# Performance work log

Measured on AMD Instinct MI355X. Metric: run time of the kernel, lower is better.

Reference implementation:

```python
import jax, jax.numpy as jnp
import numpy as np

NEG_BIG = -9e15

def setup_inputs() -> dict:
    key = jax.random.key(0)
    k1, k2, k3, k4 = jax.random.split(key, 4)
    B, N, C, D = 8, 2048, 128, 128
    x = jax.random.normal(k1, (B, N, C), dtype=jnp.float32)
    adj = jax.random.randint(k2, (N, N), 0, 2, dtype=jnp.int32)
    W = jax.random.normal(k3, (D, C), dtype=jnp.float32) * (1.0 / np.sqrt(C))
    a = jax.random.normal(k4, (1, 2 * D), dtype=jnp.float32) * (1.0 / np.sqrt(2 * D))
    return {"x": x, "adj": adj, "W": W, "a": a}

def reference(x, adj, W, a):
    # Wh: [B,N,D]
    Wh = jnp.einsum('bnc,dc->bnd', x, W)
    D = Wh.shape[-1]
    a1, a2 = a[0, :D], a[0, D:]
    # e[b,i,j] = leakyrelu(a1.Wh_i + a2.Wh_j)  (algebraic split of cat([Wh_i,Wh_j]) @ a)
    f1 = Wh @ a1  # [B,N]
    f2 = Wh @ a2  # [B,N]
    e = jax.nn.leaky_relu(f1[:, :, None] + f2[:, None, :], negative_slope=0.2)  # [B,N,N]
    e = jnp.where(adj[None] > 0, e, NEG_BIG)
    attention = jax.nn.softmax(e, axis=-1)
    h_prime = jnp.einsum('bij,bjd->bid', attention, Wh)
    return jax.nn.elu(h_prime)
```

## Files before the change

### kernel.cpp

```cpp
#include <hip/hip_runtime.h>
#include <hip/hip_bf16.h>
#include <math.h>

#define BB 8
#define NN 2048
#define CC 128
#define DD 128

typedef __attribute__((ext_vector_type(8))) short short8;
typedef __attribute__((ext_vector_type(4))) float f32x4;

static __device__ __forceinline__ unsigned short f2bf(float f) {
    __hip_bfloat16 h = __float2bfloat16(f);
    return *reinterpret_cast<unsigned short*>(&h);
}
static __device__ __forceinline__ float bf2f(unsigned short u) {
    __hip_bfloat16 h = *reinterpret_cast<__hip_bfloat16*>(&u);
    return __bfloat162float(h);
}

#define PACKB 256
__global__ __launch_bounds__(256) void prep_wh_kernel(
    const int* __restrict__ adj, unsigned int* __restrict__ padj,
    const float* __restrict__ x, const float* __restrict__ W,
    const float* __restrict__ a,
    unsigned short* __restrict__ WhbT,
    float* __restrict__ f1, unsigned int* __restrict__ EGp)
{
    __shared__ unsigned short Whs[128 * 136];
    __shared__ unsigned short Wls[128 * 136];
    const int bx  = blockIdx.x;
    const int tid = threadIdx.x;

    if (bx < PACKB) {
        const int wid = bx * 256 + tid;
        #pragma unroll
        for (int rep = 0; rep < 2; ++rep) {
            const int word = wid + rep * 65536;
            const int4* src = (const int4*)adj + (size_t)word * 8;
            unsigned int m = 0;
            #pragma unroll
            for (int k = 0; k < 8; ++k) {
                int4 v = src[k];
                m |= (v.x > 0 ? 1u : 0u) << (k * 4);
                m |= (v.y > 0 ? 1u : 0u) << (k * 4 + 1);
                m |= (v.z > 0 ? 1u : 0u) << (k * 4 + 2);
                m |= (v.w > 0 ? 1u : 0u) << (k * 4 + 3);
            }
            padj[word] = m;
        }
        return;
    }

    const int g  = bx - PACKB;
    const int b  = g & 7;
    const int n0 = (g >> 3) * 64;

    #pragma unroll
    for (int k = 0; k < 16; ++k) {
        const int e   = tid + 256 * k;
        float4 wv = *(const float4*)&W[e * 4];
        const int row = e >> 5;
        const int col = (e & 31) * 4;
        ushort4 hv, lv;
        hv.x = f2bf(wv.x); lv.x = f2bf(wv.x - bf2f(hv.x));
        hv.y = f2bf(wv.y); lv.y = f2bf(wv.y - bf2f(hv.y));
        hv.z = f2bf(wv.z); lv.z = f2bf(wv.z - bf2f(hv.z));
        hv.w = f2bf(wv.w); lv.w = f2bf(wv.w - bf2f(hv.w));
        *(ushort4*)&Whs[row * 136 + col] = hv;
        *(ushort4*)&Wls[row * 136 + col] = lv;
    }
    __syncthreads();

    const int w    = tid >> 6;
    const int lane = tid & 63;
    const int fr   = lane & 15, fk = lane >> 4;
    const int n    = n0 + w * 16 + fr;

    short8 bh[4], bl[4];
    const float* xrow = &x[((size_t)(b * NN) + n) * CC];
    #pragma unroll
    for (int ks = 0; ks < 4; ++ks) {
        float xv[8];
        *(float4*)&xv[0] = *(const float4*)&xrow[(ks * 4 + fk) * 8];
        *(float4*)&xv[4] = *(const float4*)&xrow[(ks * 4 + fk) * 8 + 4];
        #pragma unroll
        for (int e = 0; e < 8; ++e) {
            unsigned short h = f2bf(xv[e]);
            bh[ks][e] = (short)h;
            bl[ks][e] = (short)f2bf(xv[e] - bf2f(h));
        }
    }

    f32x4 acc[8];
    #pragma unroll
    for (int dt = 0; dt < 8; ++dt) acc[dt] = (f32x4){0.f, 0.f, 0.f, 0.f};

    #pragma unroll
    for (int dt = 0; dt < 8; ++dt) {
        #pragma unroll
        for (int ks = 0; ks < 4; ++ks) {
            const int off = (dt * 16 + fr) * 136 + (ks * 4 + fk) * 8;
            short8 aH = *(const short8*)&Whs[off];
            short8 aL = *(const short8*)&Wls[off];
            acc[dt] = __builtin_amdgcn_mfma_f32_16x16x32_bf16(aH, bh[ks], acc[dt], 0, 0, 0);
            acc[dt] = __builtin_amdgcn_mfma_f32_16x16x32_bf16(aH, bl[ks], acc[dt], 0, 0, 0);
            acc[dt] = __builtin_amdgcn_mfma_f32_16x16x32_bf16(aL, bh[ks], acc[dt], 0, 0, 0);
        }
    }

    float p1 = 0.f, p2 = 0.f;
    #pragma unroll
    for (int dt = 0; dt < 8; ++dt) {
        #pragma unroll
        for (int r = 0; r < 4; ++r) {
            const int d = dt * 16 + fk * 4 + r;
            p1 += acc[dt][r] * a[d];
            p2 += acc[dt][r] * a[DD + d];
        }
    }
    p1 += __shfl_xor(p1, 16); p1 += __shfl_xor(p1, 32);
    p2 += __shfl_xor(p2, 16); p2 += __shfl_xor(p2, 32);
    if (fk == 0) {
        f1[b * NN + n] = p1;
        unsigned short e2 = f2bf(__expf(p2));
        unsigned short g2 = f2bf(__expf(0.2f * p2));
        EGp[b * NN + n] = (unsigned int)e2 | ((unsigned int)g2 << 16);
    }

    #pragma unroll
    for (int dt = 0; dt < 8; ++dt) {
        #pragma unroll
        for (int r = 0; r < 4; ++r) {
            const int d = dt * 16 + fk * 4 + r;
            WhbT[((size_t)(b * 128 + d)) * NN + n] = f2bf(acc[dt][r]);
        }
    }
}

__global__ __launch_bounds__(256) void gat_kernel(
    const unsigned short* __restrict__ WhbT,
    const unsigned int* __restrict__ padj,
    const float* __restrict__ f1,
    const unsigned int* __restrict__ EGp,
    float* __restrict__ out)
{
    constexpr int NC = NN / 64;
    __shared__ __align__(16) unsigned char smem[41216];
    unsigned short* Bs0 = (unsigned short*)smem;
    unsigned short* Bs1 = (unsigned short*)(smem + 16384);
    unsigned short* Ps0 = (unsigned short*)(smem + 32768);
    unsigned short* Ps1 = (unsigned short*)(smem + 36864);
    float* Srow = (float*)(smem + 40960);
    float* Sred = (float*)(smem + 41088);
    float* T    = (float*)smem;

    const int tid  = threadIdx.x;
    const int gblk = blockIdx.x;
    const int b    = gblk & 7;
    const int i0   = (gblk >> 3) * 32;

    const int prow = tid >> 3;
    const int pjb  = tid & 7;
    const float f1r = f1[b * NN + i0 + prow];
    const float E1r = __expf(f1r);
    const float G1r = __expf(0.2f * f1r);
    const int psw = ((pjb ^ (prow & 7)) << 3);
    const unsigned int* padjRow = padj + (size_t)(i0 + prow) * 64;
    const unsigned int* egRow   = EGp + (size_t)b * NN + pjb * 8;

    const int w    = tid >> 6;
    const int lane = tid & 63;
    const int fr   = lane & 15;
    const int fk   = lane >> 4;
    f32x4 acc00 = {0.f,0.f,0.f,0.f}, acc01 = {0.f,0.f,0.f,0.f};
    f32x4 acc10 = {0.f,0.f,0.f,0.f}, acc11 = {0.f,0.f,0.f,0.f};
    float s_part = 0.f;

    const size_t wbase = (size_t)b * 128 * NN;
    const int g0 = tid,       gd0 = g0 >> 3, gj0 = (g0 & 7) * 8;
    const int g1 = tid + 256, gd1 = g1 >> 3, gj1 = (g1 & 7) * 8;
    const int g2 = tid + 512, gd2 = g2 >> 3, gj2 = (g2 & 7) * 8;
    const int g3 = tid + 768, gd3 = g3 >> 3, gj3 = (g3 & 7) * 8;
    const int sw0 = gd0 * 64 + ((((g0) & 7) ^ (gd0 & 7)) << 3);
    const int sw1 = gd1 * 64 + ((((g1) & 7) ^ (gd1 & 7)) << 3);
    const int sw2 = gd2 * 64 + ((((g2) & 7) ^ (gd2 & 7)) << 3);
    const int sw3 = gd3 * 64 + ((((g3) & 7) ^ (gd3 & 7)) << 3);

    uint4 brA0, brA1, brA2, brA3, brB0, brB1, brB2, brB3;
    uint4 egA0, egA1, egB0, egB1;
    unsigned int pwA, pwB;

#define LOADSET(s, c) do {                                                   \
        br##s##0 = *(const uint4*)&WhbT[wbase + (size_t)gd0 * NN + (c) * 64 + gj0]; \
        br##s##1 = *(const uint4*)&WhbT[wbase + (size_t)gd1 * NN + (c) * 64 + gj1]; \
        br##s##2 = *(const uint4*)&WhbT[wbase + (size_t)gd2 * NN + (c) * 64 + gj2]; \
        br##s##3 = *(const uint4*)&WhbT[wbase + (size_t)gd3 * NN + (c) * 64 + gj3]; \
        pw##s    = padjRow[(c) * 2 + (pjb >> 2)];                            \
        eg##s##0 = *(const uint4*)(egRow + (c) * 64);                        \
        eg##s##1 = *(const uint4*)(egRow + (c) * 64 + 4);                    \
    } while (0)

#define PSTAGE(Bsb, Psb, s) do {                                             \
        unsigned int egw[8];                                                 \
        *(uint4*)&egw[0] = eg##s##0; *(uint4*)&egw[4] = eg##s##1;            \
        unsigned int pbits = (pw##s >> ((pjb & 3) << 3)) & 0xffu;            \
        unsigned short pks[8];                                               \
        float ssum = 0.f;                                                    \
        _Pragma("unroll")                                                    \
        for (int e = 0; e < 8; ++e) {                                        \
            float e2 = bf2f((unsigned short)(egw[e] & 0xffffu));             \
            float g2 = bf2f((unsigned short)(egw[e] >> 16));                 \
            float mv = E1r * e2;                                             \
            float gg = G1r * g2;                                             \
            float wv = fmaxf(mv, gg);                                        \
            wv = ((pbits >> e) & 1u) ? wv : 0.f;                             \
            unsigned short bw = f2bf(wv);                                    \
            pks[e] = bw;                                                     \
            ssum += bf2f(bw);                                                \
        }                                                                    \
        s_part += ssum;                                                      \
        *(uint4*)&Bsb[sw0] = br##s##0;                                       \
        *(uint4*)&Bsb[sw1] = br##s##1;                                       \
        *(uint4*)&Bsb[sw2] = br##s##2;                                       \
        *(uint4*)&Bsb[sw3] = br##s##3;                                       \
        uint4 pv;                                                            \
        pv.x = (unsigned int)pks[0] | ((unsigned int)pks[1] << 16);          \
        pv.y = (unsigned int)pks[2] | ((unsigned int)pks[3] << 16);          \
        pv.z = (unsigned int)pks[4] | ((unsigned int)pks[5] << 16);          \
        pv.w = (unsigned int)pks[6] | ((unsigned int)pks[7] << 16);          \
        *(uint4*)&Psb[prow * 64 + psw] = pv;                                 \
    } while (0)

#define MFMAC(Bsb, Psb) do {                                                 \
        __builtin_amdgcn_s_setprio(1);                                       \
        _Pragma("unroll")                                                    \
        for (int ks = 0; ks < 2; ++ks) {                                     \
            const int jbl = ks * 4 + fk;                                     \
            const int sb  = ((jbl ^ (fr & 7)) << 3);                         \
            short8 aF0 = *(const short8*)&Psb[fr * 64 + sb];                 \
            short8 aF1 = *(const short8*)&Psb[(16 + fr) * 64 + sb];          \
            short8 bF0 = *(const short8*)&Bsb[(w * 32 + fr) * 64 + sb];      \
            short8 bF1 = *(const short8*)&Bsb[(w * 32 + 16 + fr) * 64 + sb]; \
            acc00 = __builtin_amdgcn_mfma_f32_16x16x32_bf16(aF0, bF0, acc00, 0, 0, 0); \
            acc01 = __builtin_amdgcn_mfma_f32_16x16x32_bf16(aF0, bF1, acc01, 0, 0, 0); \
            acc10 = __builtin_amdgcn_mfma_f32_16x16x32_bf16(aF1, bF0, acc10, 0, 0, 0); \
            acc11 = __builtin_amdgcn_mfma_f32_16x16x32_bf16(aF1, bF1, acc11, 0, 0, 0); \
        }                                                                    \
        __builtin_amdgcn_s_setprio(0);                                       \
    } while (0)

    LOADSET(A, 0);
    PSTAGE(Bs0, Ps0, A);
    LOADSET(B, 1);
    __syncthreads();

    #pragma unroll 1
    for (int cc = 0; cc < NC; cc += 2) {
        PSTAGE(Bs1, Ps1, B);
        if (cc + 2 < NC) LOADSET(A, cc + 2);
        MFMAC(Bs0, Ps0);
        __syncthreads();
        if (cc + 2 < NC) PSTAGE(Bs0, Ps0, A);
        if (cc + 3 < NC) LOADSET(B, cc + 3);
        MFMAC(Bs1, Ps1);
        __syncthreads();
    }

#undef LOADSET
#undef PSTAGE
#undef MFMAC

    {
        float v = s_part;
        v += __shfl_xor(v, 1); v += __shfl_xor(v, 2); v += __shfl_xor(v, 4);
        if (pjb == 0) Srow[prow] = v;
    }
    __syncthreads();
    if (tid < 32) Sred[tid] = 1.0f / Srow[tid];
    __syncthreads();

    #pragma unroll
    for (int it = 0; it < 2; ++it) {
        #pragma unroll
        for (int dt = 0; dt < 2; ++dt) {
            f32x4 av = (it == 0) ? (dt == 0 ? acc00 : acc01)
                                 : (dt == 0 ? acc10 : acc11);
            #pragma unroll
            for (int r = 0; r < 4; ++r) {
                const int i = it * 16 + fk * 4 + r;
                const int d = w * 32 + dt * 16 + fr;
                float hv = av[r] * Sred[i];
                hv = (hv > 0.f) ? hv : expm1f(hv);
                T[i * 132 + d] = hv;
            }
        }
    }
    __syncthreads();

    #pragma unroll
    for (int k = 0; k < 4; ++k) {
        const int g   = tid + 256 * k;
        const int row = g >> 5;
        const int d4  = (g & 31) * 4;
        float4 h = *(const float4*)&T[row * 132 + d4];
        *(float4*)&out[((size_t)(b * NN) + i0 + row) * DD + d4] = h;
    }
}

extern "C" void kernel_launch(void* const* d_in, const int* in_sizes, int n_in,
                              void* d_out, int out_size, void* d_ws, size_t ws_size,
                              hipStream_t stream) {
    const float* x   = (const float*)d_in[0];
    const int*   adj = (const int*)d_in[1];
    const float* W   = (const float*)d_in[2];
    const float* a   = (const float*)d_in[3];
    float* out = (float*)d_out;

    char* p = (char*)d_ws;
    unsigned short* WhbT = (unsigned short*)p; p += (size_t)BB * NN * DD * 2;
    float* f1 = (float*)p;                p += (size_t)BB * NN * 4;
    unsigned int* EGp = (unsigned int*)p; p += (size_t)BB * NN * 4;
    unsigned int* padj = (unsigned int*)p; p += (size_t)NN * 64 * 4;

    prep_wh_kernel<<<PACKB + (NN / 64) * BB, 256, 0, stream>>>(
        adj, padj, x, W, a, WhbT, f1, EGp);
    gat_kernel<<<(NN / 32) * BB, 256, 0, stream>>>(
        WhbT, padj, f1, EGp, out);
}
```

Measured before the change: 38.26 us.

## Single-buffer 128-wide chunks with EG table staged in LDS

The attention kernel now processes 128-column chunks instead of 64, using a single LDS buffer for Wh and P rather than double buffering. Two register sets of global loads stay in flight. The per-batch EG exponent table is copied into shared memory once per block instead of being read from global memory each chunk. Because PSTAGE writes and MFMA reads share one buffer, each half-iteration now needs two barriers, so the P-computation no longer overlaps the MFMA. Register pressure also rises from holding sixteen uint4 prefetch values.

```diff
diff --git a/kernel.cpp b/kernel.cpp
--- a/kernel.cpp
+++ b/kernel.cpp
@@ -145,20 +145,23 @@
     const unsigned int* __restrict__ EGp,
     float* __restrict__ out)
 {
-    constexpr int NC = NN / 64;
-    __shared__ __align__(16) unsigned char smem[41216];
-    unsigned short* Bs0 = (unsigned short*)smem;
-    unsigned short* Bs1 = (unsigned short*)(smem + 16384);
-    unsigned short* Ps0 = (unsigned short*)(smem + 32768);
-    unsigned short* Ps1 = (unsigned short*)(smem + 36864);
-    float* Srow = (float*)(smem + 40960);
-    float* Sred = (float*)(smem + 41088);
+    constexpr int NF = NN / 128;
+    __shared__ __align__(16) unsigned char smem[49408];
+    unsigned short* Bs  = (unsigned short*)smem;
+    unsigned short* Ps  = (unsigned short*)(smem + 32768);
+    unsigned int*   EGs = (unsigned int*)(smem + 40960);
+    float* Srow = (float*)(smem + 49152);
+    float* Sred = (float*)(smem + 49280);
     float* T    = (float*)smem;
 
     const int tid  = threadIdx.x;
     const int gblk = blockIdx.x;
     const int b    = gblk & 7;
     const int i0   = (gblk >> 3) * 32;
+
+    #pragma unroll
+    for (int k = 0; k < NN / 256; ++k)
+        EGs[tid + 256 * k] = EGp[b * NN + tid + 256 * k];
 
     const int prow = tid >> 3;
     const int pjb  = tid & 7;
@@ -167,7 +170,6 @@
     const float G1r = __expf(0.2f * f1r);
     const int psw = ((pjb ^ (prow & 7)) << 3);
     const unsigned int* padjRow = padj + (size_t)(i0 + prow) * 64;
-    const unsigned int* egRow   = EGp + (size_t)b * NN + pjb * 8;
 
     const int w    = tid >> 6;
     const int lane = tid & 63;
@@ -187,24 +189,29 @@
     const int sw2 = gd2 * 64 + ((((g2) & 7) ^ (gd2 & 7)) << 3);
     const int sw3 = gd3 * 64 + ((((g3) & 7) ^ (gd3 & 7)) << 3);
 
-    uint4 brA0, brA1, brA2, brA3, brB0, brB1, brB2, brB3;
-    uint4 egA0, egA1, egB0, egB1;
-    unsigned int pwA, pwB;
-
-#define LOADSET(s, c) do {                                                   \
-        br##s##0 = *(const uint4*)&WhbT[wbase + (size_t)gd0 * NN + (c) * 64 + gj0]; \
-        br##s##1 = *(const uint4*)&WhbT[wbase + (size_t)gd1 * NN + (c) * 64 + gj1]; \
-        br##s##2 = *(const uint4*)&WhbT[wbase + (size_t)gd2 * NN + (c) * 64 + gj2]; \
-        br##s##3 = *(const uint4*)&WhbT[wbase + (size_t)gd3 * NN + (c) * 64 + gj3]; \
-        pw##s    = padjRow[(c) * 2 + (pjb >> 2)];                            \
-        eg##s##0 = *(const uint4*)(egRow + (c) * 64);                        \
-        eg##s##1 = *(const uint4*)(egRow + (c) * 64 + 4);                    \
+    uint4 brA0, brA1, brA2, brA3, brA4, brA5, brA6, brA7;
+    uint4 brB0, brB1, brB2, brB3, brB4, brB5, brB6, brB7;
+    unsigned int pwA0, pwA1, pwB0, pwB1;
+
+#define LOADSET(s, c) do {            \
+        br##s##0 = *(const uint4*)&WhbT[wbase + (size_t)gd0 * NN + (2*(c)) * 64 + gj0]; \
+        br##s##1 = *(const uint4*)&WhbT[wbase + (size_t)gd1 * NN + (2*(c)) * 64 + gj1]; \
+        br##s##2 = *(const uint4*)&WhbT[wbase + (size_t)gd2 * NN + (2*(c)) * 64 + gj2]; \
+        br##s##3 = *(const uint4*)&WhbT[wbase + (size_t)gd3 * NN + (2*(c)) * 64 + gj3]; \
+        br##s##4 = *(const uint4*)&WhbT[wbase + (size_t)gd0 * NN + (2*(c)+1) * 64 + gj0]; \
+        br##s##5 = *(const uint4*)&WhbT[wbase + (size_t)gd1 * NN + (2*(c)+1) * 64 + gj1]; \
+        br##s##6 = *(const uint4*)&WhbT[wbase + (size_t)gd2 * NN + (2*(c)+1) * 64 + gj2]; \
+        br##s##7 = *(const uint4*)&WhbT[wbase + (size_t)gd3 * NN + (2*(c)+1) * 64 + gj3]; \
+        pw##s##0 = padjRow[(2*(c)) * 2 + (pjb >> 2)];                        \
+        pw##s##1 = padjRow[(2*(c)+1) * 2 + (pjb >> 2)];                      \
     } while (0)
 
-#define PSTAGE(Bsb, Psb, s) do {                                             \
+#define PHALF(pwv, bX0, bX1, bX2, bX3, sc, h) do {                           \
+        uint4 ea = *(const uint4*)&EGs[(sc) * 64 + pjb * 8];                 \
+        uint4 eb = *(const uint4*)&EGs[(sc) * 64 + pjb * 8 + 4];             \
         unsigned int egw[8];                                                 \
-        *(uint4*)&egw[0] = eg##s##0; *(uint4*)&egw[4] = eg##s##1;            \
-        unsigned int pbits = (pw##s >> ((pjb & 3) << 3)) & 0xffu;            \
+        *(uint4*)&egw[0] = ea; *(uint4*)&egw[4] = eb;                        \
+        unsigned int pbits = ((pwv) >> ((pjb & 3) << 3)) & 0xffu;            \
         unsigned short pks[8];                                               \
         float ssum = 0.f;                                                    \
         _Pragma("unroll")                                                    \
@@ -220,54 +227,64 @@
             ssum += bf2f(bw);                                                \
         }                                                                    \
         s_part += ssum;                                                      \
-        *(uint4*)&Bsb[sw0] = br##s##0;                                       \
-        *(uint4*)&Bsb[sw1] = br##s##1;                                       \
-        *(uint4*)&Bsb[sw2] = br##s##2;                                       \
-        *(uint4*)&Bsb[sw3] = br##s##3;                                       \
+        *(uint4*)&Bs[(h) * 8192 + sw0] = bX0;                                \
+        *(uint4*)&Bs[(h) * 8192 + sw1] = bX1;                                \
+        *(uint4*)&Bs[(h) * 8192 + sw2] = bX2;                                \
+        *(uint4*)&Bs[(h) * 8192 + sw3] = bX3;                                \
         uint4 pv;                                                            \
         pv.x = (unsigned int)pks[0] | ((unsigned int)pks[1] << 16);          \
         pv.y = (unsigned int)pks[2] | ((unsigned int)pks[3] << 16);          \
         pv.z = (unsigned int)pks[4] | ((unsigned int)pks[5] << 16);          \
         pv.w = (unsigned int)pks[6] | ((unsigned int)pks[7] << 16);          \
-        *(uint4*)&Psb[prow * 64 + psw] = pv;                                 \
+        *(uint4*)&Ps[(h) * 2048 + prow * 64 + psw] = pv;                     \
     } while (0)
 
-#define MFMAC(Bsb, Psb) do {                                                 \
+#define PSTAGE(s, c) do {                                                    \
+        PHALF(pw##s##0, br##s##0, br##s##1, br##s##2, br##s##3, 2*(c),     0); \
+        PHALF(pw##s##1, br##s##4, br##s##5, br##s##6, br##s##7, 2*(c) + 1, 1); \
+    } while (0)
+
+#define MFMAC() do {                                                         \
         __builtin_amdgcn_s_setprio(1);                                       \
         _Pragma("unroll")                                                    \
-        for (int ks = 0; ks < 2; ++ks) {                                     \
-            const int jbl = ks * 4 + fk;                                     \
-            const int sb  = ((jbl ^ (fr & 7)) << 3);                         \
-            short8 aF0 = *(const short8*)&Psb[fr * 64 + sb];                 \
-            short8 aF1 = *(const short8*)&Psb[(16 + fr) * 64 + sb];          \
-            short8 bF0 = *(const short8*)&Bsb[(w * 32 + fr) * 64 + sb];      \
-            short8 bF1 = *(const short8*)&Bsb[(w * 32 + 16 + fr) * 64 + sb]; \
-            acc00 = __builtin_amdgcn_mfma_f32_16x16x32_bf16(aF0, bF0, acc00, 0, 0, 0); \
-            acc01 = __builtin_amdgcn_mfma_f32_16x16x32_bf16(aF0, bF1, acc01, 0, 0, 0); \
-            acc10 = __builtin_amdgcn_mfma_f32_16x16x32_bf16(aF1, bF0, acc10, 0, 0, 0); \
-            acc11 = __builtin_amdgcn_mfma_f32_16x16x32_bf16(aF1, bF1, acc11, 0, 0, 0); \
+        for (int h = 0; h < 2; ++h) {                                        \
+            _Pragma("unroll")                                                \
+            for (int ks = 0; ks < 2; ++ks) {                                 \
+                const int jbl = ks * 4 + fk;                                 \
+                const int sb  = ((jbl ^ (fr & 7)) << 3);                     \
+                short8 aF0 = *(const short8*)&Ps[h * 2048 + fr * 64 + sb];   \
+                short8 aF1 = *(const short8*)&Ps[h * 2048 + (16 + fr) * 64 + sb]; \
+                short8 bF0 = *(const short8*)&Bs[h * 8192 + (w * 32 + fr) * 64 + sb]; \
+                short8 bF1 = *(const short8*)&Bs[h * 8192 + (w * 32 + 16 + fr) * 64 + sb]; \
+                acc00 = __builtin_amdgcn_mfma_f32_16x16x32_bf16(aF0, bF0, acc00, 0, 0, 0); \
+                acc01 = __builtin_amdgcn_mfma_f32_16x16x32_bf16(aF0, bF1, acc01, 0, 0, 0); \
+                acc10 = __builtin_amdgcn_mfma_f32_16x16x32_bf16(aF1, bF0, acc10, 0, 0, 0); \
+                acc11 = __builtin_amdgcn_mfma_f32_16x16x32_bf16(aF1, bF1, acc11, 0, 0, 0); \
+            }                                                                \
         }                                                                    \
         __builtin_amdgcn_s_setprio(0);                                       \
     } while (0)
 
     LOADSET(A, 0);
-    PSTAGE(Bs0, Ps0, A);
     LOADSET(B, 1);
     __syncthreads();
 
     #pragma unroll 1
-    for (int cc = 0; cc < NC; cc += 2) {
-        PSTAGE(Bs1, Ps1, B);
-        if (cc + 2 < NC) LOADSET(A, cc + 2);
-        MFMAC(Bs0, Ps0);
+    for (int cc = 0; cc < NF; cc += 2) {
+        PSTAGE(A, cc);
+        if (cc + 2 < NF) LOADSET(A, cc + 2);
         __syncthreads();
-        if (cc + 2 < NC) PSTAGE(Bs0, Ps0, A);
-        if (cc + 3 < NC) LOADSET(B, cc + 3);
-        MFMAC(Bs1, Ps1);
+        MFMAC();
         __syncthreads();
+        PSTAGE(B, cc + 1);
+        if (cc + 3 < NF) LOADSET(B, cc + 3);
+        __syncthreads();
+        MFMAC();
+        __syncthreads();
     }
 
 #undef LOADSET
+#undef PHALF
 #undef PSTAGE
 #undef MFMAC
 
```

Measured after the change: 40.73 us. 1.06x slower.
